# Kernel tuning notes

Measured on AMD Instinct MI355X. Metric: run time of the kernel, lower is better.

The kernel has to match this reference:

```python
import jax, jax.numpy as jnp
import numpy as np

VOCAB = 32000
MAXLEN = 512
E = 768
H = 12
D = E // H  # 64
L = 6
F = int(E * 8 / 3)  # 2048
THETA = 10000.0
EPS = 1.1920929e-07  # torch.finfo(float32).eps, RMSNorm default


def _rms_norm(x, w):
    var = jnp.mean(x * x, axis=-1, keepdims=True)
    return x * jax.lax.rsqrt(var + EPS) * w


def _rope(x, cos, sin):
    # x: [B,H,C,D]; cos/sin: [C,D/2] (interleaved even/odd convention)
    xe = x[..., 0::2]
    xo = x[..., 1::2]
    re = xe * cos - xo * sin
    ro = xe * sin + xo * cos
    out = jnp.stack([re, ro], axis=-1)  # [B,H,C,D/2,2]
    return out.reshape(x.shape)


def setup_inputs() -> dict:
    key = jax.random.key(0)
    ks = jax.random.split(key, 13)
    s = 0.02
    ids = jax.random.randint(ks[0], (8, MAXLEN), 0, VOCAB)
    embed = jax.random.normal(ks[1], (VOCAB, E), jnp.float32) * s
    norm1_w = jnp.ones((L, E), jnp.float32)
    wq = jax.random.normal(ks[2], (L, E, H * D), jnp.float32) * s
    wk = jax.random.normal(ks[3], (L, E, H * D), jnp.float32) * s
    wv = jax.random.normal(ks[4], (L, E, H * D), jnp.float32) * s
    wo = jax.random.normal(ks[5], (L, H * D, E), jnp.float32) * s
    norm2_w = jnp.ones((L, E), jnp.float32)
    w_gate = jax.random.normal(ks[6], (L, E, F), jnp.float32) * s
    w_val = jax.random.normal(ks[7], (L, E, F), jnp.float32) * s
    w_out = jax.random.normal(ks[8], (L, F, E), jnp.float32) * s
    normf_w = jnp.ones((E,), jnp.float32)
    unembed = jax.random.normal(ks[9], (E, VOCAB), jnp.float32) * s
    return {"ids": ids, "embed": embed, "norm1_w": norm1_w, "wq": wq,
            "wk": wk, "wv": wv, "wo": wo, "norm2_w": norm2_w,
            "w_gate": w_gate, "w_val": w_val, "w_out": w_out,
            "normf_w": normf_w, "unembed": unembed}


def reference(ids, embed, norm1_w, wq, wk, wv, wo, norm2_w,
              w_gate, w_val, w_out, normf_w, unembed):
    B, C = ids.shape
    # RoPE caches [C, D/2]
    half_ids = jnp.arange(D // 2, dtype=jnp.float32)
    inv_freq = 1.0 / (THETA ** (2.0 * half_ids / D))
    angles = jnp.arange(C, dtype=jnp.float32)[:, None] * inv_freq[None, :]
    cos, sin = jnp.cos(angles), jnp.sin(angles)
    causal = jnp.tril(jnp.ones((C, C), bool))

    x = embed[ids]  # [B,C,E]
    for l in range(L):
        h = _rms_norm(x, norm1_w[l])
        q = (h @ wq[l]).reshape(B, C, H, D).transpose(0, 2, 1, 3)
        k = (h @ wk[l]).reshape(B, C, H, D).transpose(0, 2, 1, 3)
        v = (h @ wv[l]).reshape(B, C, H, D).transpose(0, 2, 1, 3)
        q = _rope(q, cos, sin)
        k = _rope(k, cos, sin)
        scores = jnp.einsum('bhqd,bhkd->bhqk', q, k) / jnp.sqrt(jnp.float32(D))
        scores = jnp.where(causal, scores, -jnp.inf)
        w = jax.nn.softmax(scores, axis=-1)
        attn = jnp.einsum('bhqk,bhkd->bhqd', w, v)
        attn = attn.transpose(0, 2, 1, 3).reshape(B, C, H * D)
        x = x + attn @ wo[l]
        h2 = _rms_norm(x, norm2_w[l])
        gated = jax.nn.silu(h2 @ w_gate[l]) * (h2 @ w_val[l])
        x = x + gated @ w_out[l]
    x = _rms_norm(x, normf_w)
    return x @ unembed  # [B,C,VOCAB]
```

## Files before the change

kernel.cpp:

```cpp
#include <hip/hip_runtime.h>
#include <hip/hip_bf16.h>
#include <stdint.h>

typedef __hip_bfloat16 bf16;
typedef unsigned short ushort_t;
typedef __attribute__((ext_vector_type(8))) short bf16x8;
typedef __attribute__((ext_vector_type(4))) float f32x4;

#define EPSV 1.1920929e-07f

__device__ __forceinline__ float bfu2f(uint32_t u) {
  union { uint32_t i; float f; } t; t.i = u << 16; return t.f;
}
__device__ __forceinline__ ushort_t f2bfu(float f) {
  bf16 h = __float2bfloat16(f);
  return *reinterpret_cast<ushort_t*>(&h);
}

#define BAR() __builtin_amdgcn_s_barrier()
#define SCHEDB() __builtin_amdgcn_sched_barrier(0)
#define WAIT_LGKM0() { asm volatile("s_waitcnt lgkmcnt(0)" ::: "memory"); SCHEDB(); }
#define WAIT_VM4() asm volatile("s_waitcnt vmcnt(4)" ::: "memory")
#define WAIT_VM0() asm volatile("s_waitcnt vmcnt(0)" ::: "memory")

__global__ void rope_table_kernel(float* __restrict__ cosT, float* __restrict__ sinT) {
  int i = blockIdx.x * 256 + threadIdx.x;
  if (i >= 512 * 32) return;
  int c = i >> 5, dp = i & 31;
  float inv = powf(10000.0f, -(2.0f * dp) / 64.0f);
  float a = (float)c * inv;
  cosT[i] = cosf(a);
  sinT[i] = sinf(a);
}

__global__ __launch_bounds__(256) void embed_rms_kernel(const int* __restrict__ ids,
                                                        const float* __restrict__ emb,
                                                        const float* __restrict__ wgt,
                                                        float* __restrict__ x,
                                                        bf16* __restrict__ h) {
  const int row = blockIdx.x;
  const int tid = threadIdx.x;
  const float* er = emb + (size_t)ids[row] * 768;
  float v0 = er[tid], v1 = er[tid + 256], v2 = er[tid + 512];
  float s = v0 * v0 + v1 * v1 + v2 * v2;
#pragma unroll
  for (int d = 1; d < 64; d <<= 1) s += __shfl_xor(s, d);
  __shared__ float red[4];
  if ((tid & 63) == 0) red[tid >> 6] = s;
  __syncthreads();
  s = red[0] + red[1] + red[2] + red[3];
  float rs = rsqrtf(s * (1.0f / 768.0f) + EPSV);
  float* xr = x + (size_t)row * 768;
  bf16* hr = h + (size_t)row * 768;
  xr[tid] = v0; xr[tid + 256] = v1; xr[tid + 512] = v2;
  hr[tid]       = __float2bfloat16(v0 * rs * wgt[tid]);
  hr[tid + 256] = __float2bfloat16(v1 * rs * wgt[tid + 256]);
  hr[tid + 512] = __float2bfloat16(v2 * rs * wgt[tid + 512]);
}

template <int S>
__global__ __launch_bounds__(256) void reduce_rms_kernel(float* __restrict__ x,
                                                         const float* __restrict__ P,
                                                         const float* __restrict__ wgt,
                                                         bf16* __restrict__ h) {
  const int row = blockIdx.x;
  const int tid = threadIdx.x;
  float* xr = x + (size_t)row * 768;
  float v[3];
#pragma unroll
  for (int j = 0; j < 3; ++j) {
    int c = tid + j * 256;
    float acc = xr[c];
#pragma unroll
    for (int s = 0; s < S; ++s)
      acc += P[(size_t)s * 4096 * 768 + (size_t)row * 768 + c];
    v[j] = acc;
  }
  float s = v[0] * v[0] + v[1] * v[1] + v[2] * v[2];
#pragma unroll
  for (int d = 1; d < 64; d <<= 1) s += __shfl_xor(s, d);
  __shared__ float red[4];
  if ((tid & 63) == 0) red[tid >> 6] = s;
  __syncthreads();
  s = red[0] + red[1] + red[2] + red[3];
  float rs = rsqrtf(s * (1.0f / 768.0f) + EPSV);
  bf16* hr = h + (size_t)row * 768;
#pragma unroll
  for (int j = 0; j < 3; ++j) {
    int c = tid + j * 256;
    xr[c] = v[j];
    hr[c] = __float2bfloat16(v[j] * rs * wgt[c]);
  }
}

__global__ __launch_bounds__(256) void transpose_all_kernel(
    const float* __restrict__ wq, const float* __restrict__ wk,
    const float* __restrict__ wv, const float* __restrict__ wo,
    const float* __restrict__ wg, const float* __restrict__ wvl,
    const float* __restrict__ wout, const float* __restrict__ unemb,
    bf16* __restrict__ wqkvT, bf16* __restrict__ woT,
    bf16* __restrict__ wgvT, bf16* __restrict__ woutT,
    bf16* __restrict__ unembT) {
  int id = blockIdx.x;
  const float* src; bf16* dst; int K, N, tile;
  bool gvmode = false; int w2 = 0;
  if (id < 13824) {
    int m = id / 576; tile = id % 576;
    int l = m >> 2, w3 = m & 3;
    K = 768; N = 768;
    const float* s0 = (w3 == 0) ? wq : (w3 == 1) ? wk : (w3 == 2) ? wv : wo;
    src = s0 + (size_t)l * 768 * 768;
    dst = (w3 < 3) ? wqkvT + (size_t)l * 2304 * 768 + (size_t)w3 * 768 * 768
                   : woT + (size_t)l * 768 * 768;
  } else if (id < 32256) {
    int id2 = id - 13824; int m = id2 / 1536; tile = id2 % 1536;
    int l = m >> 1; w2 = m & 1;
    K = 768; N = 2048; gvmode = true;
    src = (w2 ? wvl : wg) + (size_t)l * 768 * 2048;
    dst = wgvT + (size_t)l * 4096 * 768;
  } else if (id < 41472) {
    int id2 = id - 32256; int l = id2 / 1536; tile = id2 % 1536;
    K = 2048; N = 768;
    src = wout + (size_t)l * 2048 * 768;
    dst = woutT + (size_t)l * 768 * 2048;
  } else {
    tile = id - 41472;
    K = 768; N = 32000;
    src = unemb; dst = unembT;
  }
  int ntn = N >> 5;
  int nt = (tile % ntn) << 5, kt = (tile / ntn) << 5;
  __shared__ float tl[32][33];
  int tx = threadIdx.x & 31, ty = threadIdx.x >> 5;
#pragma unroll
  for (int i = 0; i < 4; ++i)
    tl[ty + i * 8][tx] = src[(size_t)(kt + ty + i * 8) * N + nt + tx];
  __syncthreads();
#pragma unroll
  for (int i = 0; i < 4; ++i) {
    int n = nt + ty + i * 8;
    size_t nrow = gvmode ? (size_t)((n >> 7) * 256 + w2 * 128 + (n & 127)) : (size_t)n;
    dst[nrow * K + kt + tx] = __float2bfloat16(tl[tx][ty + i * 8]);
  }
}

__global__ __launch_bounds__(256) void gemm_bt_sk(const bf16* __restrict__ A,
                                                  const bf16* __restrict__ BT,
                                                  float* __restrict__ P,
                                                  int M, int N, int KS, int K) {
  __shared__ __align__(16) bf16 As[128 * 32];
  __shared__ __align__(16) bf16 Bs[128 * 32];
  const int tid = threadIdx.x;
  const int lane = tid & 63, w = tid >> 6;
  const int g = lane >> 4, lc = lane & 15;
  const int bm = blockIdx.y * 128, bn = blockIdx.x * 128;
  const int z = blockIdx.z;
  const int koff = z * KS;
  const int wm = (w >> 1) * 64, wn = (w & 1) * 64;

  f32x4 acc[4][4];
#pragma unroll
  for (int i = 0; i < 4; ++i)
#pragma unroll
    for (int j = 0; j < 4; ++j) acc[i][j] = (f32x4){0.f, 0.f, 0.f, 0.f};

  for (int k0 = koff; k0 < koff + KS; k0 += 32) {
    __syncthreads();
#pragma unroll
    for (int j = 0; j < 2; ++j) {
      int c = (w * 2 + j) * 64 + lane;
      int row = c >> 2, part = c & 3;
      const bf16* srcA = A + (size_t)(bm + row) * K + k0 + part * 8;
      const bf16* srcB = BT + (size_t)(bn + row) * K + k0 + part * 8;
      __builtin_amdgcn_global_load_lds((const __attribute__((address_space(1))) void*)srcA,
                                       (__attribute__((address_space(3))) void*)(As + (w * 2 + j) * 512),
                                       16, 0, 0);
      __builtin_amdgcn_global_load_lds((const __attribute__((address_space(1))) void*)srcB,
                                       (__attribute__((address_space(3))) void*)(Bs + (w * 2 + j) * 512),
                                       16, 0, 0);
    }
    __syncthreads();
    bf16x8 af[4], bfr[4];
#pragma unroll
    for (int mi = 0; mi < 4; ++mi)
      af[mi] = *(const bf16x8*)(As + (wm + mi * 16 + lc) * 32 + g * 8);
#pragma unroll
    for (int ni = 0; ni < 4; ++ni)
      bfr[ni] = *(const bf16x8*)(Bs + (wn + ni * 16 + lc) * 32 + g * 8);
#pragma unroll
    for (int mi = 0; mi < 4; ++mi)
#pragma unroll
      for (int ni = 0; ni < 4; ++ni)
        acc[mi][ni] = __builtin_amdgcn_mfma_f32_16x16x32_bf16(af[mi], bfr[ni], acc[mi][ni], 0, 0, 0);
  }

  float* Pz = P + (size_t)z * M * N;
#pragma unroll
  for (int mi = 0; mi < 4; ++mi)
#pragma unroll
    for (int ni = 0; ni < 4; ++ni)
#pragma unroll
      for (int r = 0; r < 4; ++r) {
        size_t row = (size_t)bm + wm + mi * 16 + g * 4 + r;
        size_t col = (size_t)bn + wn + ni * 16 + lc;
        Pz[row * N + col] = acc[mi][ni][r];
      }
}

template <int MODE>
__global__ __launch_bounds__(512, 2) void gemm256(const bf16* __restrict__ A,
                                                  const bf16* __restrict__ BT,
                                                  void* __restrict__ C,
                                                  int M, int N, int K,
                                                  const float* __restrict__ cosT,
                                                  const float* __restrict__ sinT) {
  __shared__ __align__(16) bf16 lds[2][4][256 * 32];

  const int tid = threadIdx.x;
  const int lane = tid & 63, w = tid >> 6;
  const int wr = w >> 2, wc = w & 3;
  const int g = lane >> 4, lc = lane & 15;

  const int nwg = gridDim.x;
  const int q = nwg >> 3;
  const int wg = ((int)blockIdx.x & 7) * q + ((int)blockIdx.x >> 3);
  const int nby = M >> 8;
  const int bx = wg / nby, by = wg % nby;
  const int bm = by << 8, bn = bx << 8;

  const bf16* Ap = A + (size_t)bm * K;
  const bf16* Bp = BT + (size_t)bn * K;

  const int soff = (lc * 64) + ((((lane >> 4) ^ ((lane >> 1) & 3)) << 4));

  auto stage_half = [&](int buf, int slab, const bf16* Base, int kcol) {
#pragma unroll
    for (int j = 0; j < 2; ++j) {
      int half_id = w * 2 + j;
      int row = half_id * 16 + (lane >> 2);
      int s_log = (lane & 3) ^ ((lane >> 3) & 3);
      const bf16* src = Base + (size_t)row * K + kcol + s_log * 8;
      bf16* dst = &lds[buf][slab][half_id * 512];
      __builtin_amdgcn_global_load_lds((const __attribute__((address_space(1))) void*)src,
                                       (__attribute__((address_space(3))) void*)dst,
                                       16, 0, 0);
    }
  };

  f32x4 acc[8][4];
#pragma unroll
  for (int i = 0; i < 8; ++i)
#pragma unroll
    for (int j = 0; j < 4; ++j) acc[i][j] = (f32x4){0.f, 0.f, 0.f, 0.f};

  const int NT = K >> 6;

  stage_half(0, 0, Ap, 0);
  stage_half(0, 1, Bp, 0);
  stage_half(0, 2, Ap, 32);
  stage_half(0, 3, Bp, 32);

  bf16x8 aF[4], bF[4];

  auto ds_A = [&](int buf, int kk, int mh) {
#pragma unroll
    for (int i = 0; i < 4; ++i) {
      int byte = (wr * 128 + mh * 64 + i * 16) * 64 + soff;
      aF[i] = *(const bf16x8*)((const char*)&lds[buf][kk * 2][0] + byte);
    }
  };
  auto ds_B = [&](int buf, int kk) {
#pragma unroll
    for (int nf = 0; nf < 4; ++nf) {
      int rb = (MODE == 3) ? ((nf < 2) ? (wc * 32 + nf * 16) : (128 + wc * 32 + (nf - 2) * 16))
                           : (wc * 64 + nf * 16);
      int byte = rb * 64 + soff;
      bF[nf] = *(const bf16x8*)((const char*)&lds[buf][kk * 2 + 1][0] + byte);
    }
  };
  auto mfma16 = [&](int mh) {
    __builtin_amdgcn_s_setprio(1);
#pragma unroll
    for (int i = 0; i < 4; ++i)
#pragma unroll
      for (int nf = 0; nf < 4; ++nf)
        acc[mh * 4 + i][nf] =
            __builtin_amdgcn_mfma_f32_16x16x32_bf16(aF[i], bF[nf], acc[mh * 4 + i][nf], 0, 0, 0);
    __builtin_amdgcn_s_setprio(0);
  };

  for (int t = 0; t < NT; ++t) {
    const int buf = t & 1;
    const bool pf = (t + 1) < NT;
    const int knext = (t + 1) << 6;

    WAIT_VM4();
    BAR(); SCHEDB();
    if (pf) stage_half(buf ^ 1, 0, Ap, knext);
    ds_A(buf, 0, 0);
    ds_B(buf, 0);
    BAR();
    WAIT_LGKM0();
    mfma16(0);

    if (pf) stage_half(buf ^ 1, 1, Bp, knext);
    ds_A(buf, 0, 1);
    BAR();
    WAIT_LGKM0();
    mfma16(1);

    if (pf) { WAIT_VM4(); } else { WAIT_VM0(); }
    BAR(); SCHEDB();
    if (pf) stage_half(buf ^ 1, 2, Ap, knext + 32);
    ds_A(buf, 1, 0);
    ds_B(buf, 1);
    BAR();
    WAIT_LGKM0();
    mfma16(0);

    if (pf) stage_half(buf ^ 1, 3, Bp, knext + 32);
    ds_A(buf, 1, 1);
    BAR();
    WAIT_LGKM0();
    mfma16(1);
  }

  if (MODE == 3) {
    bf16* act = (bf16*)C;
#pragma unroll
    for (int mf = 0; mf < 8; ++mf)
#pragma unroll
      for (int nf = 0; nf < 2; ++nf)
#pragma unroll
        for (int r = 0; r < 4; ++r) {
          size_t row = (size_t)bm + wr * 128 + mf * 16 + g * 4 + r;
          size_t col = (size_t)(bn >> 1) + wc * 32 + nf * 16 + lc;
          float gg = acc[mf][nf][r];
          float vv = acc[mf][nf + 2][r];
          float sg = gg / (1.0f + __expf(-gg));
          act[row * 2048 + col] = __float2bfloat16(sg * vv);
        }
  } else if (MODE == 4) {
#pragma unroll
    for (int mf = 0; mf < 8; ++mf)
#pragma unroll
      for (int nf = 0; nf < 4; ++nf)
#pragma unroll
        for (int r = 0; r < 4; ++r) {
          int row = bm + wr * 128 + mf * 16 + g * 4 + r;
          int col = bn + wc * 64 + nf * 16 + lc;
          float v = acc[mf][nf][r];
          float p = __shfl_xor(v, 1);
          float outv = v;
          if (col < 1536) {
            int cpos = row & 511;
            int dp = (col & 63) >> 1;
            float cs = cosT[cpos * 32 + dp], sn = sinT[cpos * 32 + dp];
            float o = (col & 1) ? (p * sn + v * cs) : (v * cs - p * sn);
            outv = (col < 768) ? o * 0.125f : o;
          }
          ((bf16*)C)[(size_t)row * N + col] = __float2bfloat16(outv);
        }
  } else {
#pragma unroll
    for (int mf = 0; mf < 8; ++mf)
#pragma unroll
      for (int nf = 0; nf < 4; ++nf)
#pragma unroll
        for (int r = 0; r < 4; ++r) {
          size_t row = (size_t)bm + wr * 128 + mf * 16 + g * 4 + r;
          size_t col = (size_t)bn + wc * 64 + nf * 16 + lc;
          float v = acc[mf][nf][r];
          if (MODE == 0) ((bf16*)C)[row * N + col] = __float2bfloat16(v);
          else           ((float*)C)[row * N + col] = v;
        }
  }
}

__global__ __launch_bounds__(256) void attn_kernel(const bf16* __restrict__ qkv,
                                                   bf16* __restrict__ out) {
  const int qt = blockIdx.x;
  const int h  = blockIdx.y;
  const int b  = blockIdx.z;
  const int tid = threadIdx.x;
  const int lane = tid & 63, w = tid >> 6;
  const int g = lane >> 4, lc = lane & 15;

  __shared__ __align__(16) bf16 Ks[64][72];
  __shared__ __align__(16) bf16 Vt[64][72];
  __shared__ __align__(16) bf16 Pl[4][32][72];

  bf16x8 qa[2][2];
#pragma unroll
  for (int mi = 0; mi < 2; ++mi)
#pragma unroll
    for (int ks = 0; ks < 2; ++ks) {
      size_t t = (size_t)b * 512 + qt * 128 + w * 32 + mi * 16 + lc;
      qa[mi][ks] = *(const bf16x8*)(qkv + t * 2304 + h * 64 + ks * 32 + g * 8);
    }

  float m_r[2][4], l_r[2][4];
  f32x4 acc_o[2][4];
#pragma unroll
  for (int mi = 0; mi < 2; ++mi)
#pragma unroll
    for (int r = 0; r < 4; ++r) { m_r[mi][r] = -1e30f; l_r[mi][r] = 0.f; }
#pragma unroll
  for (int mi = 0; mi < 2; ++mi)
#pragma unroll
    for (int ni = 0; ni < 4; ++ni) acc_o[mi][ni] = (f32x4){0.f, 0.f, 0.f, 0.f};

  const int nkt = 2 * qt + 2;
  for (int kt = 0; kt < nkt; ++kt) {
    __syncthreads();
    for (int i = 0; i < 8; ++i) {
      int pi = i * 256 + tid;
      int r = pi >> 5, dp = pi & 31;
      size_t t = (size_t)b * 512 + kt * 64 + r;
      uint32_t u = *(const uint32_t*)(qkv + t * 2304 + 768 + h * 64 + dp * 2);
      *(uint32_t*)&Ks[r][dp * 2] = u;
      uint32_t uv = *(const uint32_t*)(qkv + t * 2304 + 1536 + h * 64 + dp * 2);
      *(ushort_t*)&Vt[dp * 2][r]     = (ushort_t)(uv & 0xffffu);
      *(ushort_t*)&Vt[dp * 2 + 1][r] = (ushort_t)(uv >> 16);
    }
    __syncthreads();

    f32x4 sacc[2][4];
#pragma unroll
    for (int mi = 0; mi < 2; ++mi)
#pragma unroll
      for (int ni = 0; ni < 4; ++ni) sacc[mi][ni] = (f32x4){0.f, 0.f, 0.f, 0.f};
#pragma unroll
    for (int ni = 0; ni < 4; ++ni) {
      bf16x8 kb0 = *(const bf16x8*)&Ks[ni * 16 + lc][g * 8];
      bf16x8 kb1 = *(const bf16x8*)&Ks[ni * 16 + lc][32 + g * 8];
#pragma unroll
      for (int mi = 0; mi < 2; ++mi) {
        sacc[mi][ni] = __builtin_amdgcn_mfma_f32_16x16x32_bf16(qa[mi][0], kb0, sacc[mi][ni], 0, 0, 0);
        sacc[mi][ni] = __builtin_amdgcn_mfma_f32_16x16x32_bf16(qa[mi][1], kb1, sacc[mi][ni], 0, 0, 0);
      }
    }
    if (kt >= 2 * qt) {
#pragma unroll
      for (int mi = 0; mi < 2; ++mi)
#pragma unroll
        for (int ni = 0; ni < 4; ++ni)
#pragma unroll
          for (int r = 0; r < 4; ++r) {
            int ql = w * 32 + mi * 16 + g * 4 + r;
            int kl = ni * 16 + lc;
            if (kt * 64 + kl > qt * 128 + ql) sacc[mi][ni][r] = -1e30f;
          }
    }
#pragma unroll
    for (int mi = 0; mi < 2; ++mi) {
      float mx[4], sm[4], mn[4], sc[4];
#pragma unroll
      for (int r = 0; r < 4; ++r)
        mx[r] = fmaxf(fmaxf(sacc[mi][0][r], sacc[mi][1][r]), fmaxf(sacc[mi][2][r], sacc[mi][3][r]));
#pragma unroll
      for (int d = 1; d < 16; d <<= 1)
#pragma unroll
        for (int r = 0; r < 4; ++r) mx[r] = fmaxf(mx[r], __shfl_xor(mx[r], d));
#pragma unroll
      for (int r = 0; r < 4; ++r) {
        mn[r] = fmaxf(m_r[mi][r], mx[r]);
        sc[r] = __expf(m_r[mi][r] - mn[r]);
        sm[r] = 0.f;
      }
#pragma unroll
      for (int ni = 0; ni < 4; ++ni)
#pragma unroll
        for (int r = 0; r < 4; ++r) {
          float p = __expf(sacc[mi][ni][r] - mn[r]);
          sacc[mi][ni][r] = p;
          sm[r] += p;
        }
#pragma unroll
      for (int d = 1; d < 16; d <<= 1)
#pragma unroll
        for (int r = 0; r < 4; ++r) sm[r] += __shfl_xor(sm[r], d);
#pragma unroll
      for (int r = 0; r < 4; ++r) {
        l_r[mi][r] = l_r[mi][r] * sc[r] + sm[r];
        m_r[mi][r] = mn[r];
      }
#pragma unroll
      for (int ni = 0; ni < 4; ++ni)
#pragma unroll
        for (int r = 0; r < 4; ++r) acc_o[mi][ni][r] *= sc[r];
#pragma unroll
      for (int ni = 0; ni < 4; ++ni)
#pragma unroll
        for (int r = 0; r < 4; ++r)
          *(ushort_t*)&Pl[w][mi * 16 + g * 4 + r][ni * 16 + lc] = f2bfu(sacc[mi][ni][r]);
    }
    __syncthreads();
#pragma unroll
    for (int ks = 0; ks < 2; ++ks) {
      bf16x8 pa[2];
#pragma unroll
      for (int mi = 0; mi < 2; ++mi)
        pa[mi] = *(const bf16x8*)&Pl[w][mi * 16 + lc][ks * 32 + g * 8];
#pragma unroll
      for (int ni = 0; ni < 4; ++ni) {
        bf16x8 vb = *(const bf16x8*)&Vt[ni * 16 + lc][ks * 32 + g * 8];
#pragma unroll
        for (int mi = 0; mi < 2; ++mi)
          acc_o[mi][ni] = __builtin_amdgcn_mfma_f32_16x16x32_bf16(pa[mi], vb, acc_o[mi][ni], 0, 0, 0);
      }
    }
  }
#pragma unroll
  for (int mi = 0; mi < 2; ++mi) {
    float inv[4];
#pragma unroll
    for (int r = 0; r < 4; ++r) inv[r] = 1.0f / l_r[mi][r];
#pragma unroll
    for (int ni = 0; ni < 4; ++ni)
#pragma unroll
      for (int r = 0; r < 4; ++r) {
        size_t t = (size_t)b * 512 + qt * 128 + w * 32 + mi * 16 + g * 4 + r;
        int d = ni * 16 + lc;
        out[t * 768 + h * 64 + d] = __float2bfloat16(acc_o[mi][ni][r] * inv[r]);
      }
  }
}

extern "C" void kernel_launch(void* const* d_in, const int* in_sizes, int n_in,
                              void* d_out, int out_size, void* d_ws, size_t ws_size,
                              hipStream_t stream) {
  const int*   ids    = (const int*)d_in[0];
  const float* embedW = (const float*)d_in[1];
  const float* norm1w = (const float*)d_in[2];
  const float* wq     = (const float*)d_in[3];
  const float* wk     = (const float*)d_in[4];
  const float* wv     = (const float*)d_in[5];
  const float* wo     = (const float*)d_in[6];
  const float* norm2w = (const float*)d_in[7];
  const float* wgate  = (const float*)d_in[8];
  const float* wval   = (const float*)d_in[9];
  const float* wout   = (const float*)d_in[10];
  const float* normfw = (const float*)d_in[11];
  const float* unemb  = (const float*)d_in[12];

  char* arena = (char*)d_out;
  size_t off = 0;
  auto alloc = [&](size_t bytes) -> char* {
    char* p = arena + off;
    off += (bytes + 255) & ~(size_t)255;
    return p;
  };
  float* x       = (float*)alloc(4096ull * 768 * 4);
  bf16*  h       = (bf16*)alloc(4096ull * 768 * 2);
  bf16*  qkv     = (bf16*)alloc(4096ull * 2304 * 2);
  bf16*  attnout = (bf16*)alloc(4096ull * 768 * 2);
  bf16*  act     = (bf16*)alloc(4096ull * 2048 * 2);
  float* part    = (float*)alloc(4ull * 4096 * 768 * 4);
  float* cosT    = (float*)alloc(512 * 32 * 4);
  float* sinT    = (float*)alloc(512 * 32 * 4);
  bf16*  wqkvT   = (bf16*)alloc(6ull * 2304 * 768 * 2);
  bf16*  woT     = (bf16*)alloc(6ull * 768 * 768 * 2);
  bf16*  wgvT    = (bf16*)alloc(6ull * 4096 * 768 * 2);
  bf16*  woutT   = (bf16*)alloc(6ull * 768 * 2048 * 2);

  bf16* unembT = (bf16*)d_ws;
  bf16* hf     = (bf16*)((char*)d_ws + 32000ull * 768 * 2);

  rope_table_kernel<<<64, 256, 0, stream>>>(cosT, sinT);
  transpose_all_kernel<<<65472, 256, 0, stream>>>(wq, wk, wv, wo, wgate, wval, wout, unemb,
                                                  wqkvT, woT, wgvT, woutT, unembT);
  embed_rms_kernel<<<4096, 256, 0, stream>>>(ids, embedW, norm1w, x, h);

  for (int l = 0; l < 6; ++l) {
    gemm256<4><<<16 * 9, 512, 0, stream>>>(h, wqkvT + (size_t)l * 2304 * 768, qkv,
                                           4096, 2304, 768, cosT, sinT);
    attn_kernel<<<dim3(4, 12, 8), 256, 0, stream>>>(qkv, attnout);
    gemm_bt_sk<<<dim3(6, 32, 2), 256, 0, stream>>>(attnout, woT + (size_t)l * 768 * 768, part,
                                                   4096, 768, 384, 768);
    reduce_rms_kernel<2><<<4096, 256, 0, stream>>>(x, part, norm2w + (size_t)l * 768, h);
    gemm256<3><<<16 * 16, 512, 0, stream>>>(h, wgvT + (size_t)l * 4096 * 768, act,
                                            4096, 4096, 768, nullptr, nullptr);
    gemm_bt_sk<<<dim3(6, 32, 4), 256, 0, stream>>>(act, woutT + (size_t)l * 768 * 2048, part,
                                                   4096, 768, 512, 2048);
    if (l < 5)
      reduce_rms_kernel<4><<<4096, 256, 0, stream>>>(x, part, norm1w + (size_t)(l + 1) * 768, h);
    else
      reduce_rms_kernel<4><<<4096, 256, 0, stream>>>(x, part, normfw, hf);
  }

  gemm256<1><<<16 * 125, 512, 0, stream>>>(hf, unembT, (float*)d_out, 4096, 32000, 768,
                                           nullptr, nullptr);
}
```

Baseline: 1.495 ms.

## Use 128x256 tiled QKV GEMM and register-prefetch K/V tiles in attention

```diff
diff --git a/kernel.cpp b/kernel.cpp
--- a/kernel.cpp
+++ b/kernel.cpp
@@ -21,6 +21,7 @@
 #define SCHEDB() __builtin_amdgcn_sched_barrier(0)
 #define WAIT_LGKM0() { asm volatile("s_waitcnt lgkmcnt(0)" ::: "memory"); SCHEDB(); }
 #define WAIT_VM4() asm volatile("s_waitcnt vmcnt(4)" ::: "memory")
+#define WAIT_VM3() asm volatile("s_waitcnt vmcnt(3)" ::: "memory")
 #define WAIT_VM0() asm volatile("s_waitcnt vmcnt(0)" ::: "memory")
 
 __global__ void rope_table_kernel(float* __restrict__ cosT, float* __restrict__ sinT) {
@@ -211,9 +212,7 @@
 __global__ __launch_bounds__(512, 2) void gemm256(const bf16* __restrict__ A,
                                                   const bf16* __restrict__ BT,
                                                   void* __restrict__ C,
-                                                  int M, int N, int K,
-                                                  const float* __restrict__ cosT,
-                                                  const float* __restrict__ sinT) {
+                                                  int M, int N, int K) {
   __shared__ __align__(16) bf16 lds[2][4][256 * 32];
 
   const int tid = threadIdx.x;
@@ -340,27 +339,6 @@
           float sg = gg / (1.0f + __expf(-gg));
           act[row * 2048 + col] = __float2bfloat16(sg * vv);
         }
-  } else if (MODE == 4) {
-#pragma unroll
-    for (int mf = 0; mf < 8; ++mf)
-#pragma unroll
-      for (int nf = 0; nf < 4; ++nf)
-#pragma unroll
-        for (int r = 0; r < 4; ++r) {
-          int row = bm + wr * 128 + mf * 16 + g * 4 + r;
-          int col = bn + wc * 64 + nf * 16 + lc;
-          float v = acc[mf][nf][r];
-          float p = __shfl_xor(v, 1);
-          float outv = v;
-          if (col < 1536) {
-            int cpos = row & 511;
-            int dp = (col & 63) >> 1;
-            float cs = cosT[cpos * 32 + dp], sn = sinT[cpos * 32 + dp];
-            float o = (col & 1) ? (p * sn + v * cs) : (v * cs - p * sn);
-            outv = (col < 768) ? o * 0.125f : o;
-          }
-          ((bf16*)C)[(size_t)row * N + col] = __float2bfloat16(outv);
-        }
   } else {
 #pragma unroll
     for (int mf = 0; mf < 8; ++mf)
@@ -375,6 +353,131 @@
           else           ((float*)C)[row * N + col] = v;
         }
   }
+}
+
+__global__ __launch_bounds__(512, 2) void gemm_qkv(const bf16* __restrict__ A,
+                                                   const bf16* __restrict__ BT,
+                                                   bf16* __restrict__ C,
+                                                   int M, int N, int K,
+                                                   const float* __restrict__ cosT,
+                                                   const float* __restrict__ sinT) {
+  __shared__ __align__(16) bf16 ldsA[2][2][128 * 32];
+  __shared__ __align__(16) bf16 ldsB[2][2][256 * 32];
+
+  const int tid = threadIdx.x;
+  const int lane = tid & 63, w = tid >> 6;
+  const int wr = w >> 2, wc = w & 3;
+  const int g = lane >> 4, lc = lane & 15;
+
+  const int nwg = gridDim.x;
+  const int q = nwg >> 3;
+  const int wg = ((int)blockIdx.x & 7) * q + ((int)blockIdx.x >> 3);
+  const int nby = M >> 7;
+  const int bx = wg / nby, by = wg % nby;
+  const int bm = by << 7, bn = bx << 8;
+
+  const bf16* Ap = A + (size_t)bm * K;
+  const bf16* Bp = BT + (size_t)bn * K;
+
+  const int soff = (lc * 64) + ((((lane >> 4) ^ ((lane >> 1) & 3)) << 4));
+  const int s_log = (lane & 3) ^ ((lane >> 3) & 3);
+
+  auto stage_half = [&](int buf, int kk, int kcol) {
+    {
+      int row = w * 16 + (lane >> 2);
+      const bf16* src = Ap + (size_t)row * K + kcol + s_log * 8;
+      bf16* dst = &ldsA[buf][kk][w * 512];
+      __builtin_amdgcn_global_load_lds((const __attribute__((address_space(1))) void*)src,
+                                       (__attribute__((address_space(3))) void*)dst,
+                                       16, 0, 0);
+    }
+#pragma unroll
+    for (int j = 0; j < 2; ++j) {
+      int half_id = w * 2 + j;
+      int row = half_id * 16 + (lane >> 2);
+      const bf16* src = Bp + (size_t)row * K + kcol + s_log * 8;
+      bf16* dst = &ldsB[buf][kk][half_id * 512];
+      __builtin_amdgcn_global_load_lds((const __attribute__((address_space(1))) void*)src,
+                                       (__attribute__((address_space(3))) void*)dst,
+                                       16, 0, 0);
+    }
+  };
+
+  f32x4 acc[4][4];
+#pragma unroll
+  for (int i = 0; i < 4; ++i)
+#pragma unroll
+    for (int j = 0; j < 4; ++j) acc[i][j] = (f32x4){0.f, 0.f, 0.f, 0.f};
+
+  const int NT = K >> 6;
+  stage_half(0, 0, 0);
+  stage_half(0, 1, 32);
+
+  bf16x8 aF[4], bF[4];
+  auto ds_AB = [&](int buf, int kk) {
+#pragma unroll
+    for (int i = 0; i < 4; ++i) {
+      int byte = (wr * 64 + i * 16) * 64 + soff;
+      aF[i] = *(const bf16x8*)((const char*)&ldsA[buf][kk][0] + byte);
+    }
+#pragma unroll
+    for (int nf = 0; nf < 4; ++nf) {
+      int byte = (wc * 64 + nf * 16) * 64 + soff;
+      bF[nf] = *(const bf16x8*)((const char*)&ldsB[buf][kk][0] + byte);
+    }
+  };
+  auto mfma16 = [&]() {
+    __builtin_amdgcn_s_setprio(1);
+#pragma unroll
+    for (int i = 0; i < 4; ++i)
+#pragma unroll
+      for (int nf = 0; nf < 4; ++nf)
+        acc[i][nf] = __builtin_amdgcn_mfma_f32_16x16x32_bf16(aF[i], bF[nf], acc[i][nf], 0, 0, 0);
+    __builtin_amdgcn_s_setprio(0);
+  };
+
+  for (int t = 0; t < NT; ++t) {
+    const int buf = t & 1;
+    const bool pf = (t + 1) < NT;
+    const int knext = (t + 1) << 6;
+
+    WAIT_VM3();
+    BAR(); SCHEDB();
+    if (pf) stage_half(buf ^ 1, 0, knext);
+    ds_AB(buf, 0);
+    BAR();
+    WAIT_LGKM0();
+    mfma16();
+
+    if (pf) { WAIT_VM3(); } else { WAIT_VM0(); }
+    BAR(); SCHEDB();
+    if (pf) stage_half(buf ^ 1, 1, knext + 32);
+    ds_AB(buf, 1);
+    BAR();
+    WAIT_LGKM0();
+    mfma16();
+  }
+
+#pragma unroll
+  for (int mf = 0; mf < 4; ++mf)
+#pragma unroll
+    for (int nf = 0; nf < 4; ++nf)
+#pragma unroll
+      for (int r = 0; r < 4; ++r) {
+        int row = bm + wr * 64 + mf * 16 + g * 4 + r;
+        int col = bn + wc * 64 + nf * 16 + lc;
+        float v = acc[mf][nf][r];
+        float p = __shfl_xor(v, 1);
+        float outv = v;
+        if (col < 1536) {
+          int cpos = row & 511;
+          int dp = (col & 63) >> 1;
+          float cs = cosT[cpos * 32 + dp], sn = sinT[cpos * 32 + dp];
+          float o = (col & 1) ? (p * sn + v * cs) : (v * cs - p * sn);
+          outv = (col < 768) ? o * 0.125f : o;
+        }
+        C[(size_t)row * N + col] = __float2bfloat16(outv);
+      }
 }
 
 __global__ __launch_bounds__(256) void attn_kernel(const bf16* __restrict__ qkv,
@@ -410,20 +513,40 @@
 #pragma unroll
     for (int ni = 0; ni < 4; ++ni) acc_o[mi][ni] = (f32x4){0.f, 0.f, 0.f, 0.f};
 
+  uint32_t kreg[8], vreg[8];
   const int nkt = 2 * qt + 2;
-  for (int kt = 0; kt < nkt; ++kt) {
-    __syncthreads();
+  {
+#pragma unroll
     for (int i = 0; i < 8; ++i) {
       int pi = i * 256 + tid;
       int r = pi >> 5, dp = pi & 31;
-      size_t t = (size_t)b * 512 + kt * 64 + r;
-      uint32_t u = *(const uint32_t*)(qkv + t * 2304 + 768 + h * 64 + dp * 2);
-      *(uint32_t*)&Ks[r][dp * 2] = u;
-      uint32_t uv = *(const uint32_t*)(qkv + t * 2304 + 1536 + h * 64 + dp * 2);
-      *(ushort_t*)&Vt[dp * 2][r]     = (ushort_t)(uv & 0xffffu);
-      *(ushort_t*)&Vt[dp * 2 + 1][r] = (ushort_t)(uv >> 16);
-    }
+      size_t t = (size_t)b * 512 + 0 * 64 + r;
+      kreg[i] = *(const uint32_t*)(qkv + t * 2304 + 768 + h * 64 + dp * 2);
+      vreg[i] = *(const uint32_t*)(qkv + t * 2304 + 1536 + h * 64 + dp * 2);
+    }
+  }
+
+  for (int kt = 0; kt < nkt; ++kt) {
     __syncthreads();
+#pragma unroll
+    for (int i = 0; i < 8; ++i) {
+      int pi = i * 256 + tid;
+      int r = pi >> 5, dp = pi & 31;
+      *(uint32_t*)&Ks[r][dp * 2] = kreg[i];
+      *(ushort_t*)&Vt[dp * 2][r]     = (ushort_t)(vreg[i] & 0xffffu);
+      *(ushort_t*)&Vt[dp * 2 + 1][r] = (ushort_t)(vreg[i] >> 16);
+    }
+    __syncthreads();
+    if (kt + 1 < nkt) {
+#pragma unroll
+      for (int i = 0; i < 8; ++i) {
+        int pi = i * 256 + tid;
+        int r = pi >> 5, dp = pi & 31;
+        size_t t = (size_t)b * 512 + (kt + 1) * 64 + r;
+        kreg[i] = *(const uint32_t*)(qkv + t * 2304 + 768 + h * 64 + dp * 2);
+        vreg[i] = *(const uint32_t*)(qkv + t * 2304 + 1536 + h * 64 + dp * 2);
+      }
+    }
 
     f32x4 sacc[2][4];
 #pragma unroll
@@ -573,14 +696,14 @@
   embed_rms_kernel<<<4096, 256, 0, stream>>>(ids, embedW, norm1w, x, h);
 
   for (int l = 0; l < 6; ++l) {
-    gemm256<4><<<16 * 9, 512, 0, stream>>>(h, wqkvT + (size_t)l * 2304 * 768, qkv,
-                                           4096, 2304, 768, cosT, sinT);
+    gemm_qkv<<<32 * 9, 512, 0, stream>>>(h, wqkvT + (size_t)l * 2304 * 768, qkv,
+                                         4096, 2304, 768, cosT, sinT);
     attn_kernel<<<dim3(4, 12, 8), 256, 0, stream>>>(qkv, attnout);
     gemm_bt_sk<<<dim3(6, 32, 2), 256, 0, stream>>>(attnout, woT + (size_t)l * 768 * 768, part,
                                                    4096, 768, 384, 768);
     reduce_rms_kernel<2><<<4096, 256, 0, stream>>>(x, part, norm2w + (size_t)l * 768, h);
     gemm256<3><<<16 * 16, 512, 0, stream>>>(h, wgvT + (size_t)l * 4096 * 768, act,
-                                            4096, 4096, 768, nullptr, nullptr);
+                                            4096, 4096, 768);
     gemm_bt_sk<<<dim3(6, 32, 4), 256, 0, stream>>>(act, woutT + (size_t)l * 768 * 2048, part,
                                                    4096, 768, 512, 2048);
     if (l < 5)
@@ -589,6 +712,5 @@
       reduce_rms_kernel<4><<<4096, 256, 0, stream>>>(x, part, normfw, hf);
   }
 
-  gemm256<1><<<16 * 125, 512, 0, stream>>>(hf, unembT, (float*)d_out, 4096, 32000, 768,
-                                           nullptr, nullptr);
-}
+  gemm256<1><<<16 * 125, 512, 0, stream>>>(hf, unembT, (float*)d_out, 4096, 32000, 768);
+}
```

New measurement: 1.632 ms. +9.2%, slower.

## Store split-K partials in bf16 and merge prep kernels into one launch

Applied to the files above, without the earlier changes.

```diff
diff --git a/kernel.cpp b/kernel.cpp
--- a/kernel.cpp
+++ b/kernel.cpp
@@ -23,85 +23,52 @@
 #define WAIT_VM4() asm volatile("s_waitcnt vmcnt(4)" ::: "memory")
 #define WAIT_VM0() asm volatile("s_waitcnt vmcnt(0)" ::: "memory")
 
-__global__ void rope_table_kernel(float* __restrict__ cosT, float* __restrict__ sinT) {
-  int i = blockIdx.x * 256 + threadIdx.x;
-  if (i >= 512 * 32) return;
-  int c = i >> 5, dp = i & 31;
-  float inv = powf(10000.0f, -(2.0f * dp) / 64.0f);
-  float a = (float)c * inv;
-  cosT[i] = cosf(a);
-  sinT[i] = sinf(a);
-}
-
-__global__ __launch_bounds__(256) void embed_rms_kernel(const int* __restrict__ ids,
-                                                        const float* __restrict__ emb,
-                                                        const float* __restrict__ wgt,
-                                                        float* __restrict__ x,
-                                                        bf16* __restrict__ h) {
-  const int row = blockIdx.x;
-  const int tid = threadIdx.x;
-  const float* er = emb + (size_t)ids[row] * 768;
-  float v0 = er[tid], v1 = er[tid + 256], v2 = er[tid + 512];
-  float s = v0 * v0 + v1 * v1 + v2 * v2;
-#pragma unroll
-  for (int d = 1; d < 64; d <<= 1) s += __shfl_xor(s, d);
-  __shared__ float red[4];
-  if ((tid & 63) == 0) red[tid >> 6] = s;
-  __syncthreads();
-  s = red[0] + red[1] + red[2] + red[3];
-  float rs = rsqrtf(s * (1.0f / 768.0f) + EPSV);
-  float* xr = x + (size_t)row * 768;
-  bf16* hr = h + (size_t)row * 768;
-  xr[tid] = v0; xr[tid + 256] = v1; xr[tid + 512] = v2;
-  hr[tid]       = __float2bfloat16(v0 * rs * wgt[tid]);
-  hr[tid + 256] = __float2bfloat16(v1 * rs * wgt[tid + 256]);
-  hr[tid + 512] = __float2bfloat16(v2 * rs * wgt[tid + 512]);
-}
-
-template <int S>
-__global__ __launch_bounds__(256) void reduce_rms_kernel(float* __restrict__ x,
-                                                         const float* __restrict__ P,
-                                                         const float* __restrict__ wgt,
-                                                         bf16* __restrict__ h) {
-  const int row = blockIdx.x;
-  const int tid = threadIdx.x;
-  float* xr = x + (size_t)row * 768;
-  float v[3];
-#pragma unroll
-  for (int j = 0; j < 3; ++j) {
-    int c = tid + j * 256;
-    float acc = xr[c];
-#pragma unroll
-    for (int s = 0; s < S; ++s)
-      acc += P[(size_t)s * 4096 * 768 + (size_t)row * 768 + c];
-    v[j] = acc;
-  }
-  float s = v[0] * v[0] + v[1] * v[1] + v[2] * v[2];
-#pragma unroll
-  for (int d = 1; d < 64; d <<= 1) s += __shfl_xor(s, d);
-  __shared__ float red[4];
-  if ((tid & 63) == 0) red[tid >> 6] = s;
-  __syncthreads();
-  s = red[0] + red[1] + red[2] + red[3];
-  float rs = rsqrtf(s * (1.0f / 768.0f) + EPSV);
-  bf16* hr = h + (size_t)row * 768;
-#pragma unroll
-  for (int j = 0; j < 3; ++j) {
-    int c = tid + j * 256;
-    xr[c] = v[j];
-    hr[c] = __float2bfloat16(v[j] * rs * wgt[c]);
-  }
-}
-
-__global__ __launch_bounds__(256) void transpose_all_kernel(
+__global__ __launch_bounds__(256) void prep_all_kernel(
+    const int* __restrict__ ids, const float* __restrict__ emb,
+    const float* __restrict__ norm1w0,
     const float* __restrict__ wq, const float* __restrict__ wk,
     const float* __restrict__ wv, const float* __restrict__ wo,
     const float* __restrict__ wg, const float* __restrict__ wvl,
     const float* __restrict__ wout, const float* __restrict__ unemb,
+    float* __restrict__ cosT, float* __restrict__ sinT,
     bf16* __restrict__ wqkvT, bf16* __restrict__ woT,
     bf16* __restrict__ wgvT, bf16* __restrict__ woutT,
-    bf16* __restrict__ unembT) {
+    bf16* __restrict__ unembT,
+    float* __restrict__ x, bf16* __restrict__ h) {
   int id = blockIdx.x;
+  __shared__ float tl[32][33];
+  __shared__ float red[4];
+
+  if (id >= 65536) {
+    const int row = id - 65536;
+    const int tid = threadIdx.x;
+    const float* er = emb + (size_t)ids[row] * 768;
+    float v0 = er[tid], v1 = er[tid + 256], v2 = er[tid + 512];
+    float s = v0 * v0 + v1 * v1 + v2 * v2;
+#pragma unroll
+    for (int d = 1; d < 64; d <<= 1) s += __shfl_xor(s, d);
+    if ((tid & 63) == 0) red[tid >> 6] = s;
+    __syncthreads();
+    s = red[0] + red[1] + red[2] + red[3];
+    float rs = rsqrtf(s * (1.0f / 768.0f) + EPSV);
+    float* xr = x + (size_t)row * 768;
+    bf16* hr = h + (size_t)row * 768;
+    xr[tid] = v0; xr[tid + 256] = v1; xr[tid + 512] = v2;
+    hr[tid]       = __float2bfloat16(v0 * rs * norm1w0[tid]);
+    hr[tid + 256] = __float2bfloat16(v1 * rs * norm1w0[tid + 256]);
+    hr[tid + 512] = __float2bfloat16(v2 * rs * norm1w0[tid + 512]);
+    return;
+  }
+  if (id >= 65472) {
+    int i = (id - 65472) * 256 + threadIdx.x;
+    int c = i >> 5, dp = i & 31;
+    float inv = powf(10000.0f, -(2.0f * dp) / 64.0f);
+    float a = (float)c * inv;
+    cosT[i] = cosf(a);
+    sinT[i] = sinf(a);
+    return;
+  }
+
   const float* src; bf16* dst; int K, N, tile;
   bool gvmode = false; int w2 = 0;
   if (id < 13824) {
@@ -130,7 +97,6 @@
   }
   int ntn = N >> 5;
   int nt = (tile % ntn) << 5, kt = (tile / ntn) << 5;
-  __shared__ float tl[32][33];
   int tx = threadIdx.x & 31, ty = threadIdx.x >> 5;
 #pragma unroll
   for (int i = 0; i < 4; ++i)
@@ -144,9 +110,66 @@
   }
 }
 
+template <int S>
+__global__ __launch_bounds__(256) void reduce_rms_kernel(float* __restrict__ x,
+                                                         const bf16* __restrict__ P,
+                                                         const float* __restrict__ wgt,
+                                                         bf16* __restrict__ h) {
+  const int row = blockIdx.x;
+  const int tid = threadIdx.x;
+  float* xr = x + (size_t)row * 768;
+  const bool act2 = tid < 128;
+  const int u0 = tid, u1 = tid + 256;
+
+  float v00, v01, v10 = 0.f, v11 = 0.f;
+  float s;
+  {
+    float2 xv = *(const float2*)(xr + 2 * u0);
+    float a0 = xv.x, a1 = xv.y;
+#pragma unroll
+    for (int z = 0; z < S; ++z) {
+      uint32_t pu = *(const uint32_t*)(P + ((size_t)z * 4096 + row) * 768 + 2 * u0);
+      a0 += bfu2f(pu & 0xffffu); a1 += bfu2f(pu >> 16);
+    }
+    v00 = a0; v01 = a1;
+    s = a0 * a0 + a1 * a1;
+  }
+  if (act2) {
+    float2 xv = *(const float2*)(xr + 2 * u1);
+    float a0 = xv.x, a1 = xv.y;
+#pragma unroll
+    for (int z = 0; z < S; ++z) {
+      uint32_t pu = *(const uint32_t*)(P + ((size_t)z * 4096 + row) * 768 + 2 * u1);
+      a0 += bfu2f(pu & 0xffffu); a1 += bfu2f(pu >> 16);
+    }
+    v10 = a0; v11 = a1;
+    s += a0 * a0 + a1 * a1;
+  }
+#pragma unroll
+  for (int d = 1; d < 64; d <<= 1) s += __shfl_xor(s, d);
+  __shared__ float red[4];
+  if ((tid & 63) == 0) red[tid >> 6] = s;
+  __syncthreads();
+  s = red[0] + red[1] + red[2] + red[3];
+  float rs = rsqrtf(s * (1.0f / 768.0f) + EPSV);
+  bf16* hr = h + (size_t)row * 768;
+  {
+    *(float2*)(xr + 2 * u0) = make_float2(v00, v01);
+    uint32_t hw = (uint32_t)f2bfu(v00 * rs * wgt[2 * u0]) |
+                  ((uint32_t)f2bfu(v01 * rs * wgt[2 * u0 + 1]) << 16);
+    *(uint32_t*)(hr + 2 * u0) = hw;
+  }
+  if (act2) {
+    *(float2*)(xr + 2 * u1) = make_float2(v10, v11);
+    uint32_t hw = (uint32_t)f2bfu(v10 * rs * wgt[2 * u1]) |
+                  ((uint32_t)f2bfu(v11 * rs * wgt[2 * u1 + 1]) << 16);
+    *(uint32_t*)(hr + 2 * u1) = hw;
+  }
+}
+
 __global__ __launch_bounds__(256) void gemm_bt_sk(const bf16* __restrict__ A,
                                                   const bf16* __restrict__ BT,
-                                                  float* __restrict__ P,
+                                                  bf16* __restrict__ P,
                                                   int M, int N, int KS, int K) {
   __shared__ __align__(16) bf16 As[128 * 32];
   __shared__ __align__(16) bf16 Bs[128 * 32];
@@ -194,7 +217,7 @@
         acc[mi][ni] = __builtin_amdgcn_mfma_f32_16x16x32_bf16(af[mi], bfr[ni], acc[mi][ni], 0, 0, 0);
   }
 
-  float* Pz = P + (size_t)z * M * N;
+  bf16* Pz = P + (size_t)z * M * N;
 #pragma unroll
   for (int mi = 0; mi < 4; ++mi)
 #pragma unroll
@@ -203,7 +226,7 @@
       for (int r = 0; r < 4; ++r) {
         size_t row = (size_t)bm + wm + mi * 16 + g * 4 + r;
         size_t col = (size_t)bn + wn + ni * 16 + lc;
-        Pz[row * N + col] = acc[mi][ni][r];
+        Pz[row * N + col] = __float2bfloat16(acc[mi][ni][r]);
       }
 }
 
@@ -556,7 +579,7 @@
   bf16*  qkv     = (bf16*)alloc(4096ull * 2304 * 2);
   bf16*  attnout = (bf16*)alloc(4096ull * 768 * 2);
   bf16*  act     = (bf16*)alloc(4096ull * 2048 * 2);
-  float* part    = (float*)alloc(4ull * 4096 * 768 * 4);
+  bf16*  part    = (bf16*)alloc(4ull * 4096 * 768 * 2);
   float* cosT    = (float*)alloc(512 * 32 * 4);
   float* sinT    = (float*)alloc(512 * 32 * 4);
   bf16*  wqkvT   = (bf16*)alloc(6ull * 2304 * 768 * 2);
@@ -567,10 +590,11 @@
   bf16* unembT = (bf16*)d_ws;
   bf16* hf     = (bf16*)((char*)d_ws + 32000ull * 768 * 2);
 
-  rope_table_kernel<<<64, 256, 0, stream>>>(cosT, sinT);
-  transpose_all_kernel<<<65472, 256, 0, stream>>>(wq, wk, wv, wo, wgate, wval, wout, unemb,
-                                                  wqkvT, woT, wgvT, woutT, unembT);
-  embed_rms_kernel<<<4096, 256, 0, stream>>>(ids, embedW, norm1w, x, h);
+  prep_all_kernel<<<69632, 256, 0, stream>>>(ids, embedW, norm1w,
+                                             wq, wk, wv, wo, wgate, wval, wout, unemb,
+                                             cosT, sinT,
+                                             wqkvT, woT, wgvT, woutT, unembT,
+                                             x, h);
 
   for (int l = 0; l < 6; ++l) {
     gemm256<4><<<16 * 9, 512, 0, stream>>>(h, wqkvT + (size_t)l * 2304 * 768, qkv,
```

Result: faster. 1.446 ms (-3.2%).
